# Kernel tuning notes

Hardware: AMD Instinct MI355X
Metric: run time of the kernel (lower is better)

## Reference

```python
import jax, jax.numpy as jnp
import numpy as np

SIZE_DICT = 512
DIM_DICT = 256
TEMPERATURE = 0.5
EPS = 1e-10


def setup_inputs() -> dict:
    key = jax.random.key(0)
    k1, k2, k3 = jax.random.split(key, 3)
    bs, dim_z, W, H = 32, DIM_DICT, 32, 32
    z_from_encoder = jax.random.normal(k1, (bs, dim_z, W, H), dtype=jnp.float32)
    kappa_q = jnp.ones((1,), dtype=jnp.float32)
    codebook = jax.random.normal(k2, (SIZE_DICT, DIM_DICT), dtype=jnp.float32)
    gumbel_u = jax.random.uniform(k3, (bs * W * H, SIZE_DICT), dtype=jnp.float32)
    return {"z_from_encoder": z_from_encoder, "kappa_q": kappa_q,
            "codebook": codebook, "gumbel_u": gumbel_u, "flg_train": 1}


def reference(z_from_encoder, kappa_q, codebook, gumbel_u, flg_train):
    bs, dim_z, W, H = z_from_encoder.shape
    # [bs, dim_z, W, H] -> [bs*W*H, dim_z]
    z_flat = jnp.transpose(z_from_encoder, (0, 2, 3, 1)).reshape(-1, dim_z)
    kq = jnp.clip(kappa_q, 1e-5, 1e5)  # scalar-ish [1]
    # L2-normalize codebook rows
    cb = codebook / jnp.linalg.norm(codebook, axis=1, keepdims=True)
    # logit = -distance = kappa * <z, c>   [N, K]
    logit = kq * (z_flat @ cb.T)
    logit = logit - jnp.max(logit, axis=-1, keepdims=True)
    logit = jnp.clip(logit, -50.0, 50.0)
    probabilities = jax.nn.softmax(logit, axis=-1)
    log_probabilities = jax.nn.log_softmax(logit, axis=-1)
    # training path: gumbel-softmax relaxation
    g = -jnp.log(-jnp.log(gumbel_u + EPS) + EPS)
    encodings = jax.nn.softmax((logit + g) / TEMPERATURE, axis=-1)
    z_quantized = (encodings @ cb).reshape(bs, W, H, dim_z)
    avg_probs = jnp.mean(jax.lax.stop_gradient(probabilities), axis=0)
    z_to_decoder = jnp.transpose(z_quantized, (0, 3, 1, 2))
    kld_discrete = jnp.sum(probabilities * log_probabilities) / bs
    kld_continuous = jnp.mean(
        jnp.sum(z_from_encoder * (z_from_encoder - z_to_decoder) * kq[0],
                axis=(1, 2, 3)))
    loss = kld_discrete + kld_continuous
    avg_probs = jnp.clip(avg_probs, 1e-10, None)
    perplexity = jnp.exp(-jnp.sum(avg_probs * jnp.log(avg_probs + 1e-10)))
    return z_to_decoder, loss, perplexity
```

## Files before the change

### kernel.cpp

```cpp
#include <hip/hip_runtime.h>
#include <stdint.h>


typedef float v4f __attribute__((ext_vector_type(4)));
typedef short v8s __attribute__((ext_vector_type(8)));

#define ZA_STR 264
#define L2_STR 520

__device__ __forceinline__ uint16_t f2bf(float x) {
  uint32_t u = __float_as_uint(x);
  u = u + 0x7fffu + ((u >> 16) & 1u);
  return (uint16_t)(u >> 16);
}

__device__ __forceinline__ int pi_of(int p) {
  return ((p >> 7) << 7) + ((p & 15) << 3) + ((p >> 4) & 7);
}


__global__ __launch_bounds__(256) void vq_prep(const float* __restrict__ cb,
                                               const float* __restrict__ kappa,
                                               char* __restrict__ ws) {
  const int b = blockIdx.x, t = threadIdx.x;
  uint16_t* cbn2 = (uint16_t*)ws;
  uint16_t* cbt2 = (uint16_t*)(ws + 262144);
  float* shadow  = (float*)(ws + 524288);
  float* scal    = (float*)(ws + 557056);
  __shared__ float s_rn[8];

  const int cbase = (b & 63) << 3;
  const int cl = t >> 5, lt = t & 31;
  const int crow = (b < 64) ? (cbase + cl) : pi_of(cbase + cl);
  const float4 f0 = *(const float4*)(cb + crow * 256 + lt * 8);
  const float4 f1 = *(const float4*)(cb + crow * 256 + lt * 8 + 4);
  float s = f0.x*f0.x + f0.y*f0.y + f0.z*f0.z + f0.w*f0.w
          + f1.x*f1.x + f1.y*f1.y + f1.z*f1.z + f1.w*f1.w;
#pragma unroll
  for (int mm = 1; mm < 32; mm <<= 1) s += __shfl_xor(s, mm, 64);
  if (lt == 0) s_rn[cl] = 1.0f / sqrtf(s);
  __syncthreads();

  union { v8s v; uint16_t u[8]; } pk;
  if (b < 64) {
    const float kq = fminf(fmaxf(kappa[0], 1e-5f), 1e5f);
    const int code = cbase + cl, dch = lt;
    const float rn = s_rn[cl] * kq;
    pk.u[0] = f2bf(f0.x * rn); pk.u[1] = f2bf(f0.y * rn);
    pk.u[2] = f2bf(f0.z * rn); pk.u[3] = f2bf(f0.w * rn);
    pk.u[4] = f2bf(f1.x * rn); pk.u[5] = f2bf(f1.y * rn);
    pk.u[6] = f2bf(f1.z * rn); pk.u[7] = f2bf(f1.w * rn);
    const int w = code >> 7, ct = code & 7, mcol = (code >> 3) & 15;
    const int ks = dch >> 2, q3 = dch & 3;
    *(v8s*)(cbn2 + ((ks * 8 + ct) * 4 + w) * 512 + (q3 * 16 + mcol) * 8) = pk.v;
  } else {
    const int cgroup = b - 64, d = t;
#pragma unroll
    for (int j = 0; j < 8; j++) {
      const int code = pi_of((cgroup << 3) + j);
      pk.u[j] = f2bf(cb[code * 256 + d] * s_rn[j]);
    }
    const int cc = cgroup >> 2, qq = cgroup & 3;
    const int wd = d >> 6, nt = (d >> 4) & 3, md = d & 15;
    *(v8s*)(cbt2 + ((cc * 4 + nt) * 4 + wd) * 512 + (qq * 16 + md) * 8) = pk.v;
    if (t < 128) shadow[(cgroup << 7) + t] = 0.f;
    if (cgroup == 0 && t >= 128 && t < 131) scal[t - 128] = 0.f;
  }
}

__global__ __launch_bounds__(256, 4) void vq_main(const float* __restrict__ z,
                                                  const float* __restrict__ gum,
                                                  char* __restrict__ ws,
                                                  float* __restrict__ out) {
  __shared__ char s_A[33280];
  __shared__ float s_pm[128], s_pS[128], s_pT[128];
  __shared__ float s_M[32], s_rS[32], s_kd[32], s_red[8];
  __shared__ float s_se[128], s_ce[128];
  __shared__ float s_col[512];

  const int t = threadIdx.x;
  const int w = t >> 6, lane = t & 63, q = lane >> 4, m = lane & 15;
  const int bi = blockIdx.x, b = bi >> 5, wh0 = (bi & 31) << 5;
  const int R0 = bi << 5;

  const uint16_t* cbn2 = (const uint16_t*)ws;
  const uint16_t* cbt2 = (const uint16_t*)(ws + 262144);
  float* shadow = (float*)(ws + 524288);
  float* scal   = (float*)(ws + 557056);

  uint16_t* za  = (uint16_t*)s_A;
  uint16_t* l2s = (uint16_t*)s_A;

  {
    float zs = 0.f;
    const int whb = (t & 7) << 2, dT = t >> 3;
    const float* zb = z + ((size_t)b << 18) + wh0 + whb;
#pragma unroll
    for (int s = 0; s < 8; s++) {
      const int d = dT + (s << 5);
      const float4 v = *(const float4*)(zb + (d << 10));
      zs += v.x * v.x + v.y * v.y + v.z * v.z + v.w * v.w;
      za[(whb + 0) * ZA_STR + d] = f2bf(v.x);
      za[(whb + 1) * ZA_STR + d] = f2bf(v.y);
      za[(whb + 2) * ZA_STR + d] = f2bf(v.z);
      za[(whb + 3) * ZA_STR + d] = f2bf(v.w);
    }
#pragma unroll
    for (int mm = 1; mm < 64; mm <<= 1) zs += __shfl_xor(zs, mm, 64);
    if (lane == 0) s_red[w] = zs;
  }
  __syncthreads();
  if (t == 0) atomicAdd(&scal[1], s_red[0] + s_red[1] + s_red[2] + s_red[3]);

  v4f acc0[8], acc1[8];
#pragma unroll
  for (int i = 0; i < 8; i++) { acc0[i] = (v4f)0.f; acc1[i] = (v4f)0.f; }
  {
    const uint16_t* bp  = cbn2 + (w << 9) + (lane << 3);
    const uint16_t* a0p = za + m * ZA_STR;
    const uint16_t* a1p = za + (m + 16) * ZA_STR;
#pragma unroll
    for (int ks = 0; ks < 8; ks++) {
      const v8s a0 = *(const v8s*)(a0p + (ks << 5) + (q << 3));
      const v8s a1 = *(const v8s*)(a1p + (ks << 5) + (q << 3));
#pragma unroll
      for (int ct = 0; ct < 8; ct++) {
        const v8s bf = *(const v8s*)(bp + (((ks << 3) + ct) << 11));
        acc0[ct] = __builtin_amdgcn_mfma_f32_16x16x32_bf16(a0, bf, acc0[ct], 0, 0, 0);
        acc1[ct] = __builtin_amdgcn_mfma_f32_16x16x32_bf16(a1, bf, acc1[ct], 0, 0, 0);
      }
    }
  }

  {
    auto stats_half = [&](v4f (&acc)[8], int half) {
#pragma unroll
      for (int reg = 0; reg < 4; reg++) {
        float mx = -1e30f;
#pragma unroll
        for (int ct = 0; ct < 8; ct++) mx = fmaxf(mx, acc[ct][reg]);
#pragma unroll
        for (int mm = 1; mm < 16; mm <<= 1) mx = fmaxf(mx, __shfl_xor(mx, mm, 64));
        float S = 0.f, T = 0.f;
#pragma unroll
        for (int ct = 0; ct < 8; ct++) {
          const float d = acc[ct][reg] - mx;
          const float e = __expf(d);
          S += e; T += d * e;
        }
#pragma unroll
        for (int mm = 1; mm < 16; mm <<= 1) { S += __shfl_xor(S, mm, 64); T += __shfl_xor(T, mm, 64); }
        if (m == 0) {
          const int r = half * 16 + q * 4 + reg;
          s_pm[(w << 5) + r] = mx; s_pS[(w << 5) + r] = S; s_pT[(w << 5) + r] = T;
        }
      }
    };
    stats_half(acc0, 0);
    stats_half(acc1, 1);
  }

  union GU { float4 v[2]; float f[8]; };
  GU gA, gB;
  const float* gT = gum + (((size_t)R0 + (q << 2)) << 9) + (w << 7) + (m << 3);
  gA.v[0] = *(const float4*)(gT + 0);   gA.v[1] = *(const float4*)(gT + 4);
  gB.v[0] = *(const float4*)(gT + 512); gB.v[1] = *(const float4*)(gT + 516);

  __syncthreads();
  if (t < 32) {
    float M = s_pm[t];
    M = fmaxf(M, s_pm[32 + t]); M = fmaxf(M, s_pm[64 + t]); M = fmaxf(M, s_pm[96 + t]);
    float S = 0.f, T = 0.f;
#pragma unroll
    for (int ww = 0; ww < 4; ww++) {
      const float dm = s_pm[ww * 32 + t] - M;
      const float al = __expf(dm);
      S += s_pS[ww * 32 + t] * al;
      T += (s_pT[ww * 32 + t] + dm * s_pS[ww * 32 + t]) * al;
    }
    const float rS = 1.0f / S;
    s_M[t] = M; s_rS[t] = rS; s_kd[t] = T * rS - __logf(S);
  }
  __syncthreads();

  {
    const int c0 = w << 7;
    float colacc[8];
#pragma unroll
    for (int i = 0; i < 8; i++) colacc[i] = 0.f;
#pragma unroll
    for (int g = 0; g < 8; g++) {
      const int h = g >> 2, rg = g & 3;
      const int r = (h << 4) + (q << 2) + rg;
      const float Mr = s_M[r], rSr = s_rS[r];
      uint16_t* lrow = l2s + r * L2_STR + c0 + m;
      const GU& gu = (g & 1) ? gB : gA;
      float se = 0.f, ce = 0.f;
#pragma unroll
      for (int ct = 0; ct < 8; ct++) {
        const float a = h ? acc1[ct][rg] : acc0[ct][rg];
        const float d = fmaxf(a - Mr, -50.0f);
        const float e = __expf(d);
        colacc[ct] += e * rSr;
        const float L = 1e-10f - __logf(gu.f[ct] + 1e-10f);
        const float f = __fdividef(e, L);
        const float er = f * f;
        se += er;
        ce += er * (d + Mr);
        lrow[ct << 4] = f2bf(er);
      }
      if (g < 6) {
        const int g2 = g + 2;
        const int off = (((g2 >> 2) << 4) + (g2 & 3)) << 9;
        GU& gw = (g & 1) ? gB : gA;
        gw.v[0] = *(const float4*)(gT + off);
        gw.v[1] = *(const float4*)(gT + off + 4);
      }
#pragma unroll
      for (int mm = 1; mm < 16; mm <<= 1) {
        se += __shfl_xor(se, mm, 64);
        ce += __shfl_xor(ce, mm, 64);
      }
      if (m == 0) { s_se[(w << 5) + r] = se; s_ce[(w << 5) + r] = ce; }
    }
#pragma unroll
    for (int i = 0; i < 8; i++) {
      colacc[i] += __shfl_xor(colacc[i], 16, 64);
      colacc[i] += __shfl_xor(colacc[i], 32, 64);
    }
    if (q == 0) {
#pragma unroll
      for (int i = 0; i < 8; i++) s_col[c0 + (i << 4) + m] = colacc[i];
    }
  }
  __syncthreads();

  v4f acc2a[4], acc2b[4];
#pragma unroll
  for (int i = 0; i < 4; i++) { acc2a[i] = (v4f)0.f; acc2b[i] = (v4f)0.f; }
  {
    const uint16_t* a0p = l2s + m * L2_STR;
    const uint16_t* a1p = l2s + (m + 16) * L2_STR;
#pragma unroll
    for (int cc = 0; cc < 16; cc++) {
      const v8s a0 = *(const v8s*)(a0p + (cc << 5) + (q << 3));
      const v8s a1 = *(const v8s*)(a1p + (cc << 5) + (q << 3));
      const uint16_t* bp2 = cbt2 + (cc << 13) + (w << 9) + (lane << 3);
#pragma unroll
      for (int nt = 0; nt < 4; nt++) {
        const v8s bf = *(const v8s*)(bp2 + (nt << 11));
        acc2a[nt] = __builtin_amdgcn_mfma_f32_16x16x32_bf16(a0, bf, acc2a[nt], 0, 0, 0);
        acc2b[nt] = __builtin_amdgcn_mfma_f32_16x16x32_bf16(a1, bf, acc2b[nt], 0, 0, 0);
      }
    }
  }

  {
    float* ob = out + ((size_t)b << 18) + wh0;
    const int d0 = w << 6;
    float rsA[4], rsB[4];
#pragma unroll
    for (int reg = 0; reg < 4; reg++) {
      const int rA = q * 4 + reg, rB = 16 + rA;
      rsA[reg] = 1.0f / (s_se[rA] + s_se[32 + rA] + s_se[64 + rA] + s_se[96 + rA]);
      rsB[reg] = 1.0f / (s_se[rB] + s_se[32 + rB] + s_se[64 + rB] + s_se[96 + rB]);
    }
#pragma unroll
    for (int nt = 0; nt < 4; nt++) {
      const int d = d0 + (nt << 4) + m;
#pragma unroll
      for (int reg = 0; reg < 4; reg++) {
        ob[(d << 10) + q * 4 + reg]      = acc2a[nt][reg] * rsA[reg];
        ob[(d << 10) + 16 + q * 4 + reg] = acc2b[nt][reg] * rsB[reg];
      }
    }
  }

  {
    float* sh = shadow + ((bi & 15) << 9);
    atomicAdd(&sh[t], s_col[t]);
    atomicAdd(&sh[256 + t], s_col[256 + t]);
    if (w == 0) {
      float kd = s_kd[lane & 31];
#pragma unroll
      for (int mm = 1; mm < 64; mm <<= 1) kd += __shfl_xor(kd, mm, 64);
      if (lane == 0) atomicAdd(&scal[0], 0.5f * kd);
    }
    if (t < 32) {
      const float se = s_se[t] + s_se[32 + t] + s_se[64 + t] + s_se[96 + t];
      const float ce = s_ce[t] + s_ce[32 + t] + s_ce[64 + t] + s_ce[96 + t];
      float cr = ce / se;
#pragma unroll
      for (int mm = 1; mm < 32; mm <<= 1) cr += __shfl_xor(cr, mm, 64);
      if (t == 0) atomicAdd(&scal[2], cr);
    }
  }
}

__global__ __launch_bounds__(512) void vq_final(const float* __restrict__ kappa,
                                                char* __restrict__ ws,
                                                float* __restrict__ out) {
  __shared__ float red[8];
  const int t = threadIdx.x;
  const float* shadow = (const float*)(ws + 524288);
  const float* scal   = (const float*)(ws + 557056);
  float s = 0.f;
#pragma unroll
  for (int j = 0; j < 16; j++) s += shadow[(j << 9) + t];
  float avg = fmaxf(s * (1.0f / 32768.0f), 1e-10f);
  float term = avg * __logf(avg + 1e-10f);
#pragma unroll
  for (int mm = 1; mm < 64; mm <<= 1) term += __shfl_xor(term, mm, 64);
  if ((t & 63) == 0) red[t >> 6] = term;
  __syncthreads();
  if (t == 0) {
    float H = 0.f;
#pragma unroll
    for (int i = 0; i < 8; i++) H += red[i];
    const float perpl = __expf(-H);
    const float kq = fminf(fmaxf(kappa[0], 1e-5f), 1e5f);
    const float loss = (scal[0] + kq * scal[1] - scal[2]) * (1.0f / 32.0f);
    out[8388608] = loss;
    out[8388609] = perpl;
  }
}

extern "C" void kernel_launch(void* const* d_in, const int* in_sizes, int n_in,
                              void* d_out, int out_size, void* d_ws, size_t ws_size,
                              hipStream_t stream) {
  const float* z     = (const float*)d_in[0];
  const float* kappa = (const float*)d_in[1];
  const float* cb    = (const float*)d_in[2];
  const float* gum   = (const float*)d_in[3];
  char* ws = (char*)d_ws;
  float* out = (float*)d_out;
  hipLaunchKernelGGL(vq_prep,  dim3(128),  dim3(256), 0, stream, cb, kappa, ws);
  hipLaunchKernelGGL(vq_main,  dim3(1024), dim3(256), 0, stream, z, gum, ws, out);
  hipLaunchKernelGGL(vq_final, dim3(1),    dim3(512), 0, stream, kappa, ws, out);
}
```

Baseline: 197.0 us.

## Split each block's 32 rows across 8 waves and spread scalar atomics

New measurement: 274.2 us. +39.2%, slower.

```diff
diff --git a/kernel.cpp b/kernel.cpp
--- a/kernel.cpp
+++ b/kernel.cpp
@@ -64,24 +64,26 @@
     const int wd = d >> 6, nt = (d >> 4) & 3, md = d & 15;
     *(v8s*)(cbt2 + ((cc * 4 + nt) * 4 + wd) * 512 + (qq * 16 + md) * 8) = pk.v;
     if (t < 128) shadow[(cgroup << 7) + t] = 0.f;
-    if (cgroup == 0 && t >= 128 && t < 131) scal[t - 128] = 0.f;
-  }
-}
-
-__global__ __launch_bounds__(256, 4) void vq_main(const float* __restrict__ z,
+    if (cgroup == 0 && t >= 128 && t < 160) scal[t - 128] = 0.f;
+  }
+}
+
+__global__ __launch_bounds__(512, 8) void vq_main(const float* __restrict__ z,
                                                   const float* __restrict__ gum,
                                                   char* __restrict__ ws,
                                                   float* __restrict__ out) {
   __shared__ char s_A[33280];
   __shared__ float s_pm[128], s_pS[128], s_pT[128];
-  __shared__ float s_M[32], s_rS[32], s_kd[32], s_red[8];
   __shared__ float s_se[128], s_ce[128];
-  __shared__ float s_col[512];
+  __shared__ float s_col[1024];
+  __shared__ float s_red[8];
 
   const int t = threadIdx.x;
-  const int w = t >> 6, lane = t & 63, q = lane >> 4, m = lane & 15;
+  const int w2 = t >> 6, lane = t & 63, q = lane >> 4, m = lane & 15;
+  const int wc = w2 & 3, h = w2 >> 2;
   const int bi = blockIdx.x, b = bi >> 5, wh0 = (bi & 31) << 5;
   const int R0 = bi << 5;
+  const int slot = (bi & 7) << 2;
 
   const uint16_t* cbn2 = (const uint16_t*)ws;
   const uint16_t* cbt2 = (const uint16_t*)(ws + 262144);
@@ -96,8 +98,8 @@
     const int whb = (t & 7) << 2, dT = t >> 3;
     const float* zb = z + ((size_t)b << 18) + wh0 + whb;
 #pragma unroll
-    for (int s = 0; s < 8; s++) {
-      const int d = dT + (s << 5);
+    for (int s = 0; s < 4; s++) {
+      const int d = dT + (s << 6);
       const float4 v = *(const float4*)(zb + (d << 10));
       zs += v.x * v.x + v.y * v.y + v.z * v.z + v.w * v.w;
       za[(whb + 0) * ZA_STR + d] = f2bf(v.x);
@@ -107,121 +109,102 @@
     }
 #pragma unroll
     for (int mm = 1; mm < 64; mm <<= 1) zs += __shfl_xor(zs, mm, 64);
-    if (lane == 0) s_red[w] = zs;
-  }
-  __syncthreads();
-  if (t == 0) atomicAdd(&scal[1], s_red[0] + s_red[1] + s_red[2] + s_red[3]);
-
-  v4f acc0[8], acc1[8];
-#pragma unroll
-  for (int i = 0; i < 8; i++) { acc0[i] = (v4f)0.f; acc1[i] = (v4f)0.f; }
-  {
-    const uint16_t* bp  = cbn2 + (w << 9) + (lane << 3);
-    const uint16_t* a0p = za + m * ZA_STR;
-    const uint16_t* a1p = za + (m + 16) * ZA_STR;
+    if (lane == 0) s_red[w2] = zs;
+  }
+  __syncthreads();
+  float zsum = 0.f;
+  if (t == 0) {
+#pragma unroll
+    for (int i = 0; i < 8; i++) zsum += s_red[i];
+  }
+
+  v4f acc[8];
+#pragma unroll
+  for (int i = 0; i < 8; i++) acc[i] = (v4f)0.f;
+  {
+    const uint16_t* bp = cbn2 + (wc << 9) + (lane << 3);
+    const uint16_t* ap = za + ((h << 4) + m) * ZA_STR;
 #pragma unroll
     for (int ks = 0; ks < 8; ks++) {
-      const v8s a0 = *(const v8s*)(a0p + (ks << 5) + (q << 3));
-      const v8s a1 = *(const v8s*)(a1p + (ks << 5) + (q << 3));
+      const v8s a = *(const v8s*)(ap + (ks << 5) + (q << 3));
 #pragma unroll
       for (int ct = 0; ct < 8; ct++) {
         const v8s bf = *(const v8s*)(bp + (((ks << 3) + ct) << 11));
-        acc0[ct] = __builtin_amdgcn_mfma_f32_16x16x32_bf16(a0, bf, acc0[ct], 0, 0, 0);
-        acc1[ct] = __builtin_amdgcn_mfma_f32_16x16x32_bf16(a1, bf, acc1[ct], 0, 0, 0);
-      }
-    }
-  }
-
-  {
-    auto stats_half = [&](v4f (&acc)[8], int half) {
-#pragma unroll
-      for (int reg = 0; reg < 4; reg++) {
-        float mx = -1e30f;
-#pragma unroll
-        for (int ct = 0; ct < 8; ct++) mx = fmaxf(mx, acc[ct][reg]);
-#pragma unroll
-        for (int mm = 1; mm < 16; mm <<= 1) mx = fmaxf(mx, __shfl_xor(mx, mm, 64));
-        float S = 0.f, T = 0.f;
-#pragma unroll
-        for (int ct = 0; ct < 8; ct++) {
-          const float d = acc[ct][reg] - mx;
-          const float e = __expf(d);
-          S += e; T += d * e;
-        }
-#pragma unroll
-        for (int mm = 1; mm < 16; mm <<= 1) { S += __shfl_xor(S, mm, 64); T += __shfl_xor(T, mm, 64); }
-        if (m == 0) {
-          const int r = half * 16 + q * 4 + reg;
-          s_pm[(w << 5) + r] = mx; s_pS[(w << 5) + r] = S; s_pT[(w << 5) + r] = T;
-        }
-      }
-    };
-    stats_half(acc0, 0);
-    stats_half(acc1, 1);
-  }
-
-  union GU { float4 v[2]; float f[8]; };
-  GU gA, gB;
-  const float* gT = gum + (((size_t)R0 + (q << 2)) << 9) + (w << 7) + (m << 3);
-  gA.v[0] = *(const float4*)(gT + 0);   gA.v[1] = *(const float4*)(gT + 4);
-  gB.v[0] = *(const float4*)(gT + 512); gB.v[1] = *(const float4*)(gT + 516);
-
-  __syncthreads();
-  if (t < 32) {
-    float M = s_pm[t];
-    M = fmaxf(M, s_pm[32 + t]); M = fmaxf(M, s_pm[64 + t]); M = fmaxf(M, s_pm[96 + t]);
+        acc[ct] = __builtin_amdgcn_mfma_f32_16x16x32_bf16(a, bf, acc[ct], 0, 0, 0);
+      }
+    }
+  }
+
+#pragma unroll
+  for (int reg = 0; reg < 4; reg++) {
+    float mx = -1e30f;
+#pragma unroll
+    for (int ct = 0; ct < 8; ct++) mx = fmaxf(mx, acc[ct][reg]);
+#pragma unroll
+    for (int mm = 1; mm < 16; mm <<= 1) mx = fmaxf(mx, __shfl_xor(mx, mm, 64));
     float S = 0.f, T = 0.f;
 #pragma unroll
-    for (int ww = 0; ww < 4; ww++) {
-      const float dm = s_pm[ww * 32 + t] - M;
-      const float al = __expf(dm);
-      S += s_pS[ww * 32 + t] * al;
-      T += (s_pT[ww * 32 + t] + dm * s_pS[ww * 32 + t]) * al;
-    }
-    const float rS = 1.0f / S;
-    s_M[t] = M; s_rS[t] = rS; s_kd[t] = T * rS - __logf(S);
-  }
-  __syncthreads();
-
-  {
-    const int c0 = w << 7;
-    float colacc[8];
-#pragma unroll
-    for (int i = 0; i < 8; i++) colacc[i] = 0.f;
-#pragma unroll
-    for (int g = 0; g < 8; g++) {
-      const int h = g >> 2, rg = g & 3;
-      const int r = (h << 4) + (q << 2) + rg;
-      const float Mr = s_M[r], rSr = s_rS[r];
+    for (int ct = 0; ct < 8; ct++) {
+      const float d = acc[ct][reg] - mx;
+      const float e = __expf(d);
+      S += e; T += d * e;
+    }
+#pragma unroll
+    for (int mm = 1; mm < 16; mm <<= 1) { S += __shfl_xor(S, mm, 64); T += __shfl_xor(T, mm, 64); }
+    if (m == 0) {
+      const int r = (h << 4) + (q << 2) + reg;
+      s_pm[(wc << 5) + r] = mx; s_pS[(wc << 5) + r] = S; s_pT[(wc << 5) + r] = T;
+    }
+  }
+  __syncthreads();
+
+  const int c0 = wc << 7;
+  const int rbase = (h << 4) + (q << 2);
+  float colacc[8];
+#pragma unroll
+  for (int i = 0; i < 8; i++) colacc[i] = 0.f;
+  float kdsum = 0.f;
+  {
+    const float* gT = gum + (((size_t)(R0 + rbase)) << 9) + c0 + (m << 3);
+#pragma unroll
+    for (int g = 0; g < 4; g++) {
+      const int r = rbase + g;
+      float M = s_pm[r];
+      M = fmaxf(M, s_pm[32 + r]); M = fmaxf(M, s_pm[64 + r]); M = fmaxf(M, s_pm[96 + r]);
+      float S = 0.f, T = 0.f;
+#pragma unroll
+      for (int ww = 0; ww < 4; ww++) {
+        const float pm = s_pm[ww * 32 + r], pS = s_pS[ww * 32 + r];
+        const float dm = pm - M;
+        const float al = __expf(dm);
+        S += pS * al;
+        T += (s_pT[ww * 32 + r] + dm * pS) * al;
+      }
+      const float rS = 1.0f / S;
+      kdsum += T * rS - __logf(S);
+      union GU { float4 v[2]; float f[8]; } gu;
+      gu.v[0] = *(const float4*)(gT + (g << 9));
+      gu.v[1] = *(const float4*)(gT + (g << 9) + 4);
       uint16_t* lrow = l2s + r * L2_STR + c0 + m;
-      const GU& gu = (g & 1) ? gB : gA;
       float se = 0.f, ce = 0.f;
 #pragma unroll
       for (int ct = 0; ct < 8; ct++) {
-        const float a = h ? acc1[ct][rg] : acc0[ct][rg];
-        const float d = fmaxf(a - Mr, -50.0f);
+        const float d = fmaxf(acc[ct][g] - M, -50.0f);
         const float e = __expf(d);
-        colacc[ct] += e * rSr;
+        colacc[ct] += e * rS;
         const float L = 1e-10f - __logf(gu.f[ct] + 1e-10f);
         const float f = __fdividef(e, L);
         const float er = f * f;
         se += er;
-        ce += er * (d + Mr);
+        ce += er * (d + M);
         lrow[ct << 4] = f2bf(er);
-      }
-      if (g < 6) {
-        const int g2 = g + 2;
-        const int off = (((g2 >> 2) << 4) + (g2 & 3)) << 9;
-        GU& gw = (g & 1) ? gB : gA;
-        gw.v[0] = *(const float4*)(gT + off);
-        gw.v[1] = *(const float4*)(gT + off + 4);
       }
 #pragma unroll
       for (int mm = 1; mm < 16; mm <<= 1) {
         se += __shfl_xor(se, mm, 64);
         ce += __shfl_xor(ce, mm, 64);
       }
-      if (m == 0) { s_se[(w << 5) + r] = se; s_ce[(w << 5) + r] = ce; }
+      if (m == 0) { s_se[(wc << 5) + r] = se; s_ce[(wc << 5) + r] = ce; }
     }
 #pragma unroll
     for (int i = 0; i < 8; i++) {
@@ -230,70 +213,66 @@
     }
     if (q == 0) {
 #pragma unroll
-      for (int i = 0; i < 8; i++) s_col[c0 + (i << 4) + m] = colacc[i];
-    }
-  }
-  __syncthreads();
-
-  v4f acc2a[4], acc2b[4];
-#pragma unroll
-  for (int i = 0; i < 4; i++) { acc2a[i] = (v4f)0.f; acc2b[i] = (v4f)0.f; }
-  {
-    const uint16_t* a0p = l2s + m * L2_STR;
-    const uint16_t* a1p = l2s + (m + 16) * L2_STR;
+      for (int i = 0; i < 8; i++) s_col[(h << 9) + c0 + (i << 4) + m] = colacc[i];
+    }
+  }
+  __syncthreads();
+
+  v4f acc2[4];
+#pragma unroll
+  for (int i = 0; i < 4; i++) acc2[i] = (v4f)0.f;
+  {
+    const uint16_t* a2p = l2s + ((h << 4) + m) * L2_STR;
 #pragma unroll
     for (int cc = 0; cc < 16; cc++) {
-      const v8s a0 = *(const v8s*)(a0p + (cc << 5) + (q << 3));
-      const v8s a1 = *(const v8s*)(a1p + (cc << 5) + (q << 3));
-      const uint16_t* bp2 = cbt2 + (cc << 13) + (w << 9) + (lane << 3);
+      const v8s a = *(const v8s*)(a2p + (cc << 5) + (q << 3));
+      const uint16_t* bp2 = cbt2 + (cc << 13) + (wc << 9) + (lane << 3);
 #pragma unroll
       for (int nt = 0; nt < 4; nt++) {
         const v8s bf = *(const v8s*)(bp2 + (nt << 11));
-        acc2a[nt] = __builtin_amdgcn_mfma_f32_16x16x32_bf16(a0, bf, acc2a[nt], 0, 0, 0);
-        acc2b[nt] = __builtin_amdgcn_mfma_f32_16x16x32_bf16(a1, bf, acc2b[nt], 0, 0, 0);
-      }
-    }
-  }
-
-  {
-    float* ob = out + ((size_t)b << 18) + wh0;
-    const int d0 = w << 6;
-    float rsA[4], rsB[4];
+        acc2[nt] = __builtin_amdgcn_mfma_f32_16x16x32_bf16(a, bf, acc2[nt], 0, 0, 0);
+      }
+    }
+  }
+
+  {
+    float rs[4];
 #pragma unroll
     for (int reg = 0; reg < 4; reg++) {
-      const int rA = q * 4 + reg, rB = 16 + rA;
-      rsA[reg] = 1.0f / (s_se[rA] + s_se[32 + rA] + s_se[64 + rA] + s_se[96 + rA]);
-      rsB[reg] = 1.0f / (s_se[rB] + s_se[32 + rB] + s_se[64 + rB] + s_se[96 + rB]);
-    }
+      const int r = rbase + reg;
+      rs[reg] = 1.0f / (s_se[r] + s_se[32 + r] + s_se[64 + r] + s_se[96 + r]);
+    }
+    float* ob = out + ((size_t)b << 18) + wh0 + (h << 4);
 #pragma unroll
     for (int nt = 0; nt < 4; nt++) {
-      const int d = d0 + (nt << 4) + m;
-#pragma unroll
-      for (int reg = 0; reg < 4; reg++) {
-        ob[(d << 10) + q * 4 + reg]      = acc2a[nt][reg] * rsA[reg];
-        ob[(d << 10) + 16 + q * 4 + reg] = acc2b[nt][reg] * rsB[reg];
-      }
+      const int d = (wc << 6) + (nt << 4) + m;
+#pragma unroll
+      for (int reg = 0; reg < 4; reg++)
+        ob[(d << 10) + (q << 2) + reg] = acc2[nt][reg] * rs[reg];
     }
   }
 
   {
     float* sh = shadow + ((bi & 15) << 9);
-    atomicAdd(&sh[t], s_col[t]);
-    atomicAdd(&sh[256 + t], s_col[256 + t]);
-    if (w == 0) {
-      float kd = s_kd[lane & 31];
-#pragma unroll
-      for (int mm = 1; mm < 64; mm <<= 1) kd += __shfl_xor(kd, mm, 64);
-      if (lane == 0) atomicAdd(&scal[0], 0.5f * kd);
-    }
-    if (t < 32) {
-      const float se = s_se[t] + s_se[32 + t] + s_se[64 + t] + s_se[96 + t];
-      const float ce = s_ce[t] + s_ce[32 + t] + s_ce[64 + t] + s_ce[96 + t];
-      float cr = ce / se;
-#pragma unroll
-      for (int mm = 1; mm < 32; mm <<= 1) cr += __shfl_xor(cr, mm, 64);
-      if (t == 0) atomicAdd(&scal[2], cr);
-    }
+    atomicAdd(&sh[t], s_col[t] + s_col[512 + t]);
+    if (wc == 0) {
+      float v = (m == 0) ? kdsum : 0.f;
+      v += __shfl_xor(v, 16, 64);
+      v += __shfl_xor(v, 32, 64);
+      if (lane == 0) atomicAdd(&scal[slot + 0], 0.5f * v);
+    }
+    if (w2 == 0) {
+      float cr = 0.f;
+      if (lane < 32) {
+        const float se = s_se[lane] + s_se[32 + lane] + s_se[64 + lane] + s_se[96 + lane];
+        const float ce = s_ce[lane] + s_ce[32 + lane] + s_ce[64 + lane] + s_ce[96 + lane];
+        cr = ce / se;
+      }
+#pragma unroll
+      for (int mm = 1; mm < 64; mm <<= 1) cr += __shfl_xor(cr, mm, 64);
+      if (lane == 0) atomicAdd(&scal[slot + 2], cr);
+    }
+    if (t == 0) atomicAdd(&scal[slot + 1], zsum);
   }
 }
 
@@ -317,10 +296,14 @@
     float H = 0.f;
 #pragma unroll
     for (int i = 0; i < 8; i++) H += red[i];
+    float s0 = 0.f, s1 = 0.f, s2 = 0.f;
+#pragma unroll
+    for (int k = 0; k < 8; k++) {
+      s0 += scal[(k << 2) + 0]; s1 += scal[(k << 2) + 1]; s2 += scal[(k << 2) + 2];
+    }
     const float perpl = __expf(-H);
     const float kq = fminf(fmaxf(kappa[0], 1e-5f), 1e5f);
-    const float loss = (scal[0] + kq * scal[1] - scal[2]) * (1.0f / 32.0f);
-    out[8388608] = loss;
+    out[8388608] = (s0 + kq * s1 - s2) * (1.0f / 32.0f);
     out[8388609] = perpl;
   }
 }
@@ -335,6 +318,6 @@
   char* ws = (char*)d_ws;
   float* out = (float*)d_out;
   hipLaunchKernelGGL(vq_prep,  dim3(128),  dim3(256), 0, stream, cb, kappa, ws);
-  hipLaunchKernelGGL(vq_main,  dim3(1024), dim3(256), 0, stream, z, gum, ws, out);
+  hipLaunchKernelGGL(vq_main,  dim3(1024), dim3(512), 0, stream, z, gum, ws, out);
   hipLaunchKernelGGL(vq_final, dim3(1),    dim3(512), 0, stream, kappa, ws, out);
 }
```
